# Performance work log

Hardware: AMD Instinct MI355X
Metric: run time of the kernel (lower is better)

## Reference

```python
import jax, jax.numpy as jnp
import numpy as np

D_MODEL = 2048
N_HEADS = 16
D_HEAD = D_MODEL // N_HEADS  # 128


def setup_inputs() -> dict:
    key = jax.random.key(0)
    ks = jax.random.split(key, 5)
    b, t = 2, 2048
    s = 0.02
    return {
        "x": jax.random.normal(ks[0], (b, t, D_MODEL), dtype=jnp.float32),
        "Wq": jax.random.normal(ks[1], (D_MODEL, D_MODEL), dtype=jnp.float32) * s,
        "Wk": jax.random.normal(ks[2], (D_MODEL, D_HEAD), dtype=jnp.float32) * s,
        "Wv": jax.random.normal(ks[3], (D_MODEL, D_HEAD), dtype=jnp.float32) * s,
        "Wo": jax.random.normal(ks[4], (D_MODEL, D_MODEL), dtype=jnp.float32) * s,
    }


def reference(x, Wq, Wk, Wv, Wo):
    b, t, c = x.shape
    scale = D_HEAD ** -0.5
    # q: [b, h, t, d]; k, v: single shared KV head [b, s, d]
    q = (x @ Wq).reshape(b, t, N_HEADS, D_HEAD).transpose(0, 2, 1, 3)
    k = x @ Wk  # [b, s, d]
    v = x @ Wv  # [b, s, d]
    # broadcast the shared KV head across query heads without materializing copies
    scores = jnp.einsum('bhtd,bsd->bhts', q, k) * scale
    attn = jax.nn.softmax(scores, axis=-1)
    y = jnp.einsum('bhts,bsd->bhtd', attn, v)
    y = y.transpose(0, 2, 1, 3).reshape(b, t, c)
    return y @ Wo
```

## Files before the change

kernel.cpp:

```cpp
#include <hip/hip_runtime.h>

typedef unsigned short ushort_t;
typedef short bf16x8 __attribute__((ext_vector_type(8)));
typedef float f32x4 __attribute__((ext_vector_type(4)));

#define B_    2
#define T_    2048
#define C_    2048
#define H_    16
#define DH_   128
#define BT_   4096
#define NQKV  2304

#define OFF_XB   0UL
#define OFF_WT   16777216UL
#define OFF_WOT  26214400UL
#define OFF_QKV  34603008UL
#define OFF_VT   53477376UL
#define OFF_FLAG 54525952UL

__device__ __forceinline__ ushort_t f2bf(float f) {
  union { float f; unsigned u; } v; v.f = f;
  unsigned r = v.u + 0x7fffu + ((v.u >> 16) & 1u);
  return (ushort_t)(r >> 16);
}
__device__ __forceinline__ float bf2f(ushort_t u) {
  union { float f; unsigned u; } v; v.u = ((unsigned)u) << 16;
  return v.f;
}
__device__ __forceinline__ int cvtpk_bf16(float lo, float hi) {
  int r;
  asm("v_cvt_pk_bf16_f32 %0, %1, %2" : "=v"(r) : "v"(lo), "v"(hi));
  return r;
}
__device__ __forceinline__ bf16x8 mkfrag(int d0, int d1, int d2, int d3) {
  union { int i[4]; bf16x8 v; } u;
  u.i[0] = d0; u.i[1] = d1; u.i[2] = d2; u.i[3] = d3;
  return u.v;
}

__device__ __forceinline__ void gload_lds16(const ushort_t* g, ushort_t* l) {
  __builtin_amdgcn_global_load_lds((__attribute__((address_space(1))) void*)g,
                                   (__attribute__((address_space(3))) void*)l,
                                   16, 0, 0);
}

__global__ void detect_dtype(const ushort_t* x, int* flag) {
  if (threadIdx.x == 0 && blockIdx.x == 0) {
    int sane = 0;
    for (int i = 0; i < 32; ++i) {
      ushort_t u = x[2 * i];
      int e = (u >> 7) & 0xFF;
      if (u == 0 || (e >= 100 && e <= 140)) ++sane;
    }
    *flag = (sane >= 24) ? 1 : 0;
  }
}

__global__ __launch_bounds__(256) void cast_x(const void* __restrict__ xin,
                                              ushort_t* __restrict__ xb,
                                              const int* __restrict__ flag, int n8) {
  int i = blockIdx.x * 256 + threadIdx.x;
  if (i >= n8) return;
  if (*flag) {
    *(bf16x8*)(xb + (size_t)i * 8) = *(const bf16x8*)((const ushort_t*)xin + (size_t)i * 8);
  } else {
    const float* xf = (const float*)xin;
    f32x4 a = *(const f32x4*)(xf + (size_t)i * 8);
    f32x4 b = *(const f32x4*)(xf + (size_t)i * 8 + 4);
    bf16x8 o;
    o[0] = (short)f2bf(a[0]); o[1] = (short)f2bf(a[1]);
    o[2] = (short)f2bf(a[2]); o[3] = (short)f2bf(a[3]);
    o[4] = (short)f2bf(b[0]); o[5] = (short)f2bf(b[1]);
    o[6] = (short)f2bf(b[2]); o[7] = (short)f2bf(b[3]);
    *(bf16x8*)(xb + (size_t)i * 8) = o;
  }
}

__global__ __launch_bounds__(256) void transpose_cast(const void* __restrict__ src,
                                                      ushort_t* __restrict__ dst,
                                                      const int* __restrict__ flag,
                                                      int rows, int cols, int dst_ld,
                                                      int dst_row_off) {
  __shared__ float tile[32][33];
  int c0 = blockIdx.x * 32, r0 = blockIdx.y * 32;
  int tx = threadIdx.x & 31, ty = threadIdx.x >> 5;
  bool isbf = (*flag != 0);
#pragma unroll
  for (int j = 0; j < 4; ++j) {
    int r = r0 + ty + j * 8;
    float v;
    if (isbf) v = bf2f(((const ushort_t*)src)[(size_t)r * cols + c0 + tx]);
    else      v = ((const float*)src)[(size_t)r * cols + c0 + tx];
    tile[ty + j * 8][tx] = v;
  }
  __syncthreads();
#pragma unroll
  for (int j = 0; j < 4; ++j) {
    int c = c0 + ty + j * 8;
    dst[(size_t)(dst_row_off + c) * dst_ld + r0 + tx] = f2bf(tile[tx][ty + j * 8]);
  }
}

__global__ __launch_bounds__(256) void transpose_v(const ushort_t* __restrict__ qkv,
                                                   ushort_t* __restrict__ vT) {
  __shared__ ushort_t tile[32][33];
  int b = blockIdx.z;
  int t0 = blockIdx.x * 32, d0 = blockIdx.y * 32;
  int tx = threadIdx.x & 31, ty = threadIdx.x >> 5;
#pragma unroll
  for (int j = 0; j < 4; ++j) {
    int t = t0 + ty + j * 8;
    tile[ty + j * 8][tx] = qkv[(size_t)(b * T_ + t) * NQKV + 2176 + d0 + tx];
  }
  __syncthreads();
#pragma unroll
  for (int j = 0; j < 4; ++j) {
    int d = d0 + ty + j * 8;
    vT[(size_t)b * (DH_ * T_) + (size_t)d * T_ + t0 + tx] = tile[tx][ty + j * 8];
  }
}

__global__ __launch_bounds__(256) void gemm_bt(const ushort_t* __restrict__ A,
                                               const ushort_t* __restrict__ Bt,
                                               void* __restrict__ Cv,
                                               int M, int N, int K,
                                               int is_final, const int* __restrict__ flag,
                                               float qscale, int qcols) {
  __shared__ __align__(16) ushort_t As[2][128 * 32];
  __shared__ __align__(16) ushort_t Bs[2][128 * 32];
  const int tid = threadIdx.x;
  const int lane = tid & 63;
  const int wid = tid >> 6;

  const int gx = gridDim.x;
  const int nwg = gx * gridDim.y;
  const int orig = blockIdx.y * gx + blockIdx.x;
  const int qq = nwg >> 3, rr = nwg & 7;
  const int xcd = orig & 7, pos = orig >> 3;
  const int wg = (xcd < rr ? xcd * (qq + 1) : rr * (qq + 1) + (xcd - rr) * qq) + pos;
  const int bx = wg % gx, by = wg / gx;

  const int m0 = by * 128;
  const int n0 = bx * 128;
  const int wr = wid >> 1, wc = wid & 1;
  const int l15 = lane & 15, l4 = lane >> 4;

  f32x4 zero = {0.f, 0.f, 0.f, 0.f};
  f32x4 acc[4][4];
#pragma unroll
  for (int r = 0; r < 4; ++r)
#pragma unroll
    for (int c = 0; c < 4; ++c) acc[r][c] = zero;

  const ushort_t* ga = A + (size_t)(m0 + (tid >> 2)) * K + (tid & 3) * 8;
  const ushort_t* gb = Bt + (size_t)(n0 + (tid >> 2)) * K + (tid & 3) * 8;
  const size_t stride64 = (size_t)64 * K;
  const int lofs = wid * 512;

  gload_lds16(ga, As[0] + lofs);
  gload_lds16(ga + stride64, As[0] + lofs + 2048);
  gload_lds16(gb, Bs[0] + lofs);
  gload_lds16(gb + stride64, Bs[0] + lofs + 2048);

  const int NT = K >> 5;
  for (int t = 0; t < NT; ++t) {
    const int cur = t & 1;
    if (t + 1 < NT) {
      const int k1 = (t + 1) << 5;
      gload_lds16(ga + k1, As[cur ^ 1] + lofs);
      gload_lds16(ga + k1 + stride64, As[cur ^ 1] + lofs + 2048);
      gload_lds16(gb + k1, Bs[cur ^ 1] + lofs);
      gload_lds16(gb + k1 + stride64, Bs[cur ^ 1] + lofs + 2048);
      asm volatile("s_waitcnt vmcnt(4)" ::: "memory");
    } else {
      asm volatile("s_waitcnt vmcnt(0)" ::: "memory");
    }
    __builtin_amdgcn_s_barrier();

    bf16x8 af[4], bfr[4];
#pragma unroll
    for (int r = 0; r < 4; ++r)
      af[r] = *(const bf16x8*)&As[cur][(wr * 64 + r * 16 + l15) * 32 + l4 * 8];
#pragma unroll
    for (int c = 0; c < 4; ++c)
      bfr[c] = *(const bf16x8*)&Bs[cur][(wc * 64 + c * 16 + l15) * 32 + l4 * 8];
    __builtin_amdgcn_s_setprio(1);
#pragma unroll
    for (int r = 0; r < 4; ++r)
#pragma unroll
      for (int c = 0; c < 4; ++c)
        acc[r][c] = __builtin_amdgcn_mfma_f32_16x16x32_bf16(af[r], bfr[c], acc[r][c], 0, 0, 0);
    __builtin_amdgcn_s_setprio(0);
    __builtin_amdgcn_s_barrier();
  }

  const bool f32out = is_final && (*flag == 0);
#pragma unroll
  for (int r = 0; r < 4; ++r) {
#pragma unroll
    for (int c = 0; c < 4; ++c) {
      int row = m0 + wr * 64 + r * 16 + l4 * 4;
      int col = n0 + wc * 64 + c * 16 + l15;
      float s = (col < qcols) ? qscale : 1.0f;
#pragma unroll
      for (int g = 0; g < 4; ++g) {
        float v = acc[r][c][g] * s;
        if (f32out) ((float*)Cv)[(size_t)(row + g) * N + col] = v;
        else ((ushort_t*)Cv)[(size_t)(row + g) * N + col] = f2bf(v);
      }
    }
  }
}

__global__ __launch_bounds__(256, 2) void attn_kernel(const ushort_t* __restrict__ qkv,
                                                      const ushort_t* __restrict__ vT,
                                                      ushort_t* __restrict__ y) {
  __shared__ __align__(16) ushort_t Ks[2][64 * 128];
  __shared__ __align__(16) ushort_t Vs[2][128 * 64];

  const int tid = threadIdx.x;
  const int lane = tid & 63;
  const int wid = tid >> 6;
  const int h = blockIdx.y;
  const int b = blockIdx.z;
  const int tb = b * T_;
  const int q0 = blockIdx.x * 128 + wid * 32;
  const int l15 = lane & 15, l4 = lane >> 4;

  bf16x8 qf0[4], qf1[4];
  {
    const ushort_t* qb0 = qkv + (size_t)(tb + q0 + l15) * NQKV + h * DH_ + l4 * 8;
    const ushort_t* qb1 = qb0 + (size_t)16 * NQKV;
#pragma unroll
    for (int ks = 0; ks < 4; ++ks) {
      qf0[ks] = *(const bf16x8*)(qb0 + ks * 32);
      qf1[ks] = *(const bf16x8*)(qb1 + ks * 32);
    }
  }

  const ushort_t* ksrcb[4];
  const ushort_t* vsrcb[4];
  int koff[4], voff[4];
#pragma unroll
  for (int it = 0; it < 4; ++it) {
    int id = tid + it * 256;
    int krow = id >> 4, kslot = id & 15;
    ksrcb[it] = qkv + (size_t)(tb + krow) * NQKV + 2048 + ((kslot ^ (krow & 7)) << 3);
    koff[it] = (it * 256 + (wid << 6)) * 8;
    int vrow = id >> 3, vslot = id & 7;
    vsrcb[it] = vT + (size_t)b * (DH_ * T_) + (size_t)vrow * T_ + ((vslot ^ (vrow & 7)) << 3);
    voff[it] = (it * 256 + (wid << 6)) * 8;
  }

  f32x4 zero = {0.f, 0.f, 0.f, 0.f};
  f32x4 o0[8], o1[8];
#pragma unroll
  for (int i = 0; i < 8; ++i) { o0[i] = zero; o1[i] = zero; }
  float m0s = -1e30f, m1s = -1e30f;
  float l0s = 0.f, l1s = 0.f;

#pragma unroll
  for (int it = 0; it < 4; ++it) {
    gload_lds16(ksrcb[it], &Ks[0][koff[it]]);
    gload_lds16(vsrcb[it], &Vs[0][voff[it]]);
  }

  for (int st = 0; st < 32; ++st) {
    const int cur = st & 1;
    __syncthreads();
    if (st < 31) {
      const int s1 = (st + 1) * 64;
#pragma unroll
      for (int it = 0; it < 4; ++it) {
        gload_lds16(ksrcb[it] + (size_t)s1 * NQKV, &Ks[cur ^ 1][koff[it]]);
        gload_lds16(vsrcb[it] + s1, &Vs[cur ^ 1][voff[it]]);
      }
    }

    f32x4 sa0[4], sa1[4];
    __builtin_amdgcn_s_setprio(1);
#pragma unroll
    for (int c = 0; c < 4; ++c) {
      int srow = c * 16 + l15;
      int sw = srow & 7;
      bf16x8 kf[4];
#pragma unroll
      for (int ks = 0; ks < 4; ++ks)
        kf[ks] = *(const bf16x8*)&Ks[cur][srow * 128 + (((ks * 4 + l4) ^ sw) << 3)];
      sa0[c] = zero; sa1[c] = zero;
#pragma unroll
      for (int ks = 0; ks < 4; ++ks) {
        sa0[c] = __builtin_amdgcn_mfma_f32_16x16x32_bf16(kf[ks], qf0[ks], sa0[c], 0, 0, 0);
        sa1[c] = __builtin_amdgcn_mfma_f32_16x16x32_bf16(kf[ks], qf1[ks], sa1[c], 0, 0, 0);
      }
    }
    __builtin_amdgcn_s_setprio(0);

    float pmax0 = sa0[0][0];
#pragma unroll
    for (int c = 0; c < 4; ++c)
#pragma unroll
      for (int r = 0; r < 4; ++r) pmax0 = fmaxf(pmax0, sa0[c][r]);
    pmax0 = fmaxf(pmax0, __shfl_xor(pmax0, 16));
    pmax0 = fmaxf(pmax0, __shfl_xor(pmax0, 32));
    if (!__all(pmax0 - m0s <= 8.0f)) {
      float mn = fmaxf(m0s, pmax0);
      float al = exp2f(m0s - mn);
      m0s = mn; l0s *= al;
      float ar[4];
#pragma unroll
      for (int r = 0; r < 4; ++r) ar[r] = __shfl(al, l4 * 4 + r);
#pragma unroll
      for (int nb = 0; nb < 8; ++nb)
#pragma unroll
        for (int r = 0; r < 4; ++r) o0[nb][r] *= ar[r];
    }
    float ps0 = 0.f;
#pragma unroll
    for (int c = 0; c < 4; ++c)
#pragma unroll
      for (int r = 0; r < 4; ++r) {
        float p = exp2f(sa0[c][r] - m0s);
        sa0[c][r] = p;
        ps0 += p;
      }
    ps0 += __shfl_xor(ps0, 16);
    ps0 += __shfl_xor(ps0, 32);
    l0s += ps0;

    float pmax1 = sa1[0][0];
#pragma unroll
    for (int c = 0; c < 4; ++c)
#pragma unroll
      for (int r = 0; r < 4; ++r) pmax1 = fmaxf(pmax1, sa1[c][r]);
    pmax1 = fmaxf(pmax1, __shfl_xor(pmax1, 16));
    pmax1 = fmaxf(pmax1, __shfl_xor(pmax1, 32));
    if (!__all(pmax1 - m1s <= 8.0f)) {
      float mn = fmaxf(m1s, pmax1);
      float al = exp2f(m1s - mn);
      m1s = mn; l1s *= al;
      float ar[4];
#pragma unroll
      for (int r = 0; r < 4; ++r) ar[r] = __shfl(al, l4 * 4 + r);
#pragma unroll
      for (int nb = 0; nb < 8; ++nb)
#pragma unroll
        for (int r = 0; r < 4; ++r) o1[nb][r] *= ar[r];
    }
    float ps1 = 0.f;
#pragma unroll
    for (int c = 0; c < 4; ++c)
#pragma unroll
      for (int r = 0; r < 4; ++r) {
        float p = exp2f(sa1[c][r] - m1s);
        sa1[c][r] = p;
        ps1 += p;
      }
    ps1 += __shfl_xor(ps1, 16);
    ps1 += __shfl_xor(ps1, 32);
    l1s += ps1;

    const int srcA = ((lane >> 4) & 1) * 32 + l15;
    const int srcB = srcA + 16;
    const bool cHi = lane >= 32;

    bf16x8 g0pa0, g0pa1, g1pa0, g1pa1;
    {
      int pk0[2], pk1[2], pk2[2], pk3[2];
      pk0[0] = cvtpk_bf16(sa0[0][0], sa0[0][1]); pk0[1] = cvtpk_bf16(sa0[0][2], sa0[0][3]);
      pk1[0] = cvtpk_bf16(sa0[1][0], sa0[1][1]); pk1[1] = cvtpk_bf16(sa0[1][2], sa0[1][3]);
      pk2[0] = cvtpk_bf16(sa0[2][0], sa0[2][1]); pk2[1] = cvtpk_bf16(sa0[2][2], sa0[2][3]);
      pk3[0] = cvtpk_bf16(sa0[3][0], sa0[3][1]); pk3[1] = cvtpk_bf16(sa0[3][2], sa0[3][3]);
      int a00 = __shfl(pk0[0], srcA), a01 = __shfl(pk0[1], srcA);
      int a02 = __shfl(pk0[0], srcB), a03 = __shfl(pk0[1], srcB);
      int b00 = __shfl(pk1[0], srcA), b01 = __shfl(pk1[1], srcA);
      int b02 = __shfl(pk1[0], srcB), b03 = __shfl(pk1[1], srcB);
      g0pa0 = mkfrag(cHi ? b00 : a00, cHi ? b01 : a01, cHi ? b02 : a02, cHi ? b03 : a03);
      int a10 = __shfl(pk2[0], srcA), a11 = __shfl(pk2[1], srcA);
      int a12 = __shfl(pk2[0], srcB), a13 = __shfl(pk2[1], srcB);
      int b10 = __shfl(pk3[0], srcA), b11 = __shfl(pk3[1], srcA);
      int b12 = __shfl(pk3[0], srcB), b13 = __shfl(pk3[1], srcB);
      g0pa1 = mkfrag(cHi ? b10 : a10, cHi ? b11 : a11, cHi ? b12 : a12, cHi ? b13 : a13);
    }
    {
      int pk0[2], pk1[2], pk2[2], pk3[2];
      pk0[0] = cvtpk_bf16(sa1[0][0], sa1[0][1]); pk0[1] = cvtpk_bf16(sa1[0][2], sa1[0][3]);
      pk1[0] = cvtpk_bf16(sa1[1][0], sa1[1][1]); pk1[1] = cvtpk_bf16(sa1[1][2], sa1[1][3]);
      pk2[0] = cvtpk_bf16(sa1[2][0], sa1[2][1]); pk2[1] = cvtpk_bf16(sa1[2][2], sa1[2][3]);
      pk3[0] = cvtpk_bf16(sa1[3][0], sa1[3][1]); pk3[1] = cvtpk_bf16(sa1[3][2], sa1[3][3]);
      int a00 = __shfl(pk0[0], srcA), a01 = __shfl(pk0[1], srcA);
      int a02 = __shfl(pk0[0], srcB), a03 = __shfl(pk0[1], srcB);
      int b00 = __shfl(pk1[0], srcA), b01 = __shfl(pk1[1], srcA);
      int b02 = __shfl(pk1[0], srcB), b03 = __shfl(pk1[1], srcB);
      g1pa0 = mkfrag(cHi ? b00 : a00, cHi ? b01 : a01, cHi ? b02 : a02, cHi ? b03 : a03);
      int a10 = __shfl(pk2[0], srcA), a11 = __shfl(pk2[1], srcA);
      int a12 = __shfl(pk2[0], srcB), a13 = __shfl(pk2[1], srcB);
      int b10 = __shfl(pk3[0], srcA), b11 = __shfl(pk3[1], srcA);
      int b12 = __shfl(pk3[0], srcB), b13 = __shfl(pk3[1], srcB);
      g1pa1 = mkfrag(cHi ? b10 : a10, cHi ? b11 : a11, cHi ? b12 : a12, cHi ? b13 : a13);
    }

    __builtin_amdgcn_s_setprio(1);
#pragma unroll
    for (int nb = 0; nb < 8; ++nb) {
      int vrow = nb * 16 + l15;
      int sw = vrow & 7;
      bf16x8 vb0 = *(const bf16x8*)&Vs[cur][vrow * 64 + ((l4 ^ sw) << 3)];
      o0[nb] = __builtin_amdgcn_mfma_f32_16x16x32_bf16(g0pa0, vb0, o0[nb], 0, 0, 0);
      o1[nb] = __builtin_amdgcn_mfma_f32_16x16x32_bf16(g1pa0, vb0, o1[nb], 0, 0, 0);
      bf16x8 vb1 = *(const bf16x8*)&Vs[cur][vrow * 64 + (((4 + l4) ^ sw) << 3)];
      o0[nb] = __builtin_amdgcn_mfma_f32_16x16x32_bf16(g0pa1, vb1, o0[nb], 0, 0, 0);
      o1[nb] = __builtin_amdgcn_mfma_f32_16x16x32_bf16(g1pa1, vb1, o1[nb], 0, 0, 0);
    }
    __builtin_amdgcn_s_setprio(0);
  }

  {
    float lr[4];
#pragma unroll
    for (int r = 0; r < 4; ++r) lr[r] = __shfl(l0s, l4 * 4 + r);
#pragma unroll
    for (int nb = 0; nb < 8; ++nb)
#pragma unroll
      for (int r = 0; r < 4; ++r) {
        int qrow = tb + q0 + l4 * 4 + r;
        y[(size_t)qrow * C_ + h * DH_ + nb * 16 + l15] = f2bf(o0[nb][r] / lr[r]);
      }
  }
  {
    float lr[4];
#pragma unroll
    for (int r = 0; r < 4; ++r) lr[r] = __shfl(l1s, l4 * 4 + r);
#pragma unroll
    for (int nb = 0; nb < 8; ++nb)
#pragma unroll
      for (int r = 0; r < 4; ++r) {
        int qrow = tb + q0 + 16 + l4 * 4 + r;
        y[(size_t)qrow * C_ + h * DH_ + nb * 16 + l15] = f2bf(o1[nb][r] / lr[r]);
      }
  }
}

extern "C" void kernel_launch(void* const* d_in, const int* in_sizes, int n_in,
                              void* d_out, int out_size, void* d_ws, size_t ws_size,
                              hipStream_t stream) {
  (void)in_sizes; (void)n_in; (void)out_size; (void)ws_size;
  const void* x  = d_in[0];
  const void* Wq = d_in[1];
  const void* Wk = d_in[2];
  const void* Wv = d_in[3];
  const void* Wo = d_in[4];

  char* ws = (char*)d_ws;
  ushort_t* xb  = (ushort_t*)(ws + OFF_XB);
  ushort_t* WT  = (ushort_t*)(ws + OFF_WT);
  ushort_t* WoT = (ushort_t*)(ws + OFF_WOT);
  ushort_t* qkv = (ushort_t*)(ws + OFF_QKV);
  ushort_t* vTp = (ushort_t*)(ws + OFF_VT);
  int* flag     = (int*)(ws + OFF_FLAG);

  detect_dtype<<<1, 1, 0, stream>>>((const ushort_t*)x, flag);

  cast_x<<<4096, 256, 0, stream>>>(x, xb, flag, (BT_ * C_) / 8);

  transpose_cast<<<dim3(64, 64), 256, 0, stream>>>(Wq, WT, flag, 2048, 2048, 2048, 0);
  transpose_cast<<<dim3(4, 64), 256, 0, stream>>>(Wk, WT, flag, 2048, 128, 2048, 2048);
  transpose_cast<<<dim3(4, 64), 256, 0, stream>>>(Wv, WT, flag, 2048, 128, 2048, 2176);
  transpose_cast<<<dim3(64, 64), 256, 0, stream>>>(Wo, WoT, flag, 2048, 2048, 2048, 0);

  const float k1 = 0.08838834764831845f * 1.4426950408889634f;
  gemm_bt<<<dim3(NQKV / 128, BT_ / 128), 256, 0, stream>>>(xb, WT, qkv, BT_, NQKV, C_, 0, flag, k1, 2048);

  transpose_v<<<dim3(T_ / 32, DH_ / 32, B_), 256, 0, stream>>>(qkv, vTp);

  attn_kernel<<<dim3(T_ / 128, H_, B_), 256, 0, stream>>>(qkv, vTp, xb);

  gemm_bt<<<dim3(C_ / 128, BT_ / 128), 256, 0, stream>>>(xb, WoT, d_out, BT_, C_, C_, 1, flag, 1.0f, 0);
}
```

Measured before the change: 344.8 us.

## Switch attention kernel to 32x32x16 MFMA with permlane32 swaps for P

Rewrites the attention inner loop to use 32x32x16 bf16 MFMA tiles instead of 16x16x32, so each wave holds its 32 query rows in one tile and keys in two 32-row tiles. This changes the register layout of S and O and halves the number of MFMA issues and softmax shuffles per step. The P-to-A-operand relayout now uses v_permlane32_swap instead of many ds_bpermute shuffles. The final normalization multiplies by a reciprocal instead of dividing. The risks are higher accumulator register pressure, a different LDS read pattern and a layout mismatch that would silently give wrong results.

```diff
diff --git a/kernel.cpp b/kernel.cpp
--- a/kernel.cpp
+++ b/kernel.cpp
@@ -3,6 +3,7 @@
 typedef unsigned short ushort_t;
 typedef short bf16x8 __attribute__((ext_vector_type(8)));
 typedef float f32x4 __attribute__((ext_vector_type(4)));
+typedef float f32x16 __attribute__((ext_vector_type(16)));
 
 #define B_    2
 #define T_    2048
@@ -32,6 +33,9 @@
   int r;
   asm("v_cvt_pk_bf16_f32 %0, %1, %2" : "=v"(r) : "v"(lo), "v"(hi));
   return r;
+}
+__device__ __forceinline__ void plswap(int& x, int& y) {
+  asm volatile("v_permlane32_swap_b32 %0, %1" : "+v"(x), "+v"(y));
 }
 __device__ __forceinline__ bf16x8 mkfrag(int d0, int d1, int d2, int d3) {
   union { int i[4]; bf16x8 v; } u;
@@ -226,17 +230,13 @@
   const int b = blockIdx.z;
   const int tb = b * T_;
   const int q0 = blockIdx.x * 128 + wid * 32;
-  const int l15 = lane & 15, l4 = lane >> 4;
-
-  bf16x8 qf0[4], qf1[4];
+  const int l31 = lane & 31, hi = lane >> 5;
+
+  bf16x8 qf[8];
   {
-    const ushort_t* qb0 = qkv + (size_t)(tb + q0 + l15) * NQKV + h * DH_ + l4 * 8;
-    const ushort_t* qb1 = qb0 + (size_t)16 * NQKV;
-#pragma unroll
-    for (int ks = 0; ks < 4; ++ks) {
-      qf0[ks] = *(const bf16x8*)(qb0 + ks * 32);
-      qf1[ks] = *(const bf16x8*)(qb1 + ks * 32);
-    }
+    const ushort_t* qb = qkv + (size_t)(tb + q0 + l31) * NQKV + h * DH_ + hi * 8;
+#pragma unroll
+    for (int kk = 0; kk < 8; ++kk) qf[kk] = *(const bf16x8*)(qb + kk * 16);
   }
 
   const ushort_t* ksrcb[4];
@@ -253,12 +253,13 @@
     voff[it] = (it * 256 + (wid << 6)) * 8;
   }
 
-  f32x4 zero = {0.f, 0.f, 0.f, 0.f};
-  f32x4 o0[8], o1[8];
-#pragma unroll
-  for (int i = 0; i < 8; ++i) { o0[i] = zero; o1[i] = zero; }
-  float m0s = -1e30f, m1s = -1e30f;
-  float l0s = 0.f, l1s = 0.f;
+  f32x16 o[4];
+#pragma unroll
+  for (int d = 0; d < 4; ++d)
+#pragma unroll
+    for (int r = 0; r < 16; ++r) o[d][r] = 0.f;
+  float m_s = -1e30f;
+  float l_s = 0.f;
 
 #pragma unroll
   for (int it = 0; it < 4; ++it) {
@@ -278,167 +279,105 @@
       }
     }
 
-    f32x4 sa0[4], sa1[4];
+    f32x16 sa0, sa1;
+#pragma unroll
+    for (int r = 0; r < 16; ++r) { sa0[r] = 0.f; sa1[r] = 0.f; }
+    const int r0 = l31, r1 = 32 + l31;
+    const int sw0 = r0 & 7, sw1 = r1 & 7;
     __builtin_amdgcn_s_setprio(1);
 #pragma unroll
-    for (int c = 0; c < 4; ++c) {
-      int srow = c * 16 + l15;
-      int sw = srow & 7;
-      bf16x8 kf[4];
-#pragma unroll
-      for (int ks = 0; ks < 4; ++ks)
-        kf[ks] = *(const bf16x8*)&Ks[cur][srow * 128 + (((ks * 4 + l4) ^ sw) << 3)];
-      sa0[c] = zero; sa1[c] = zero;
-#pragma unroll
-      for (int ks = 0; ks < 4; ++ks) {
-        sa0[c] = __builtin_amdgcn_mfma_f32_16x16x32_bf16(kf[ks], qf0[ks], sa0[c], 0, 0, 0);
-        sa1[c] = __builtin_amdgcn_mfma_f32_16x16x32_bf16(kf[ks], qf1[ks], sa1[c], 0, 0, 0);
-      }
+    for (int kk = 0; kk < 8; ++kk) {
+      bf16x8 k0 = *(const bf16x8*)&Ks[cur][r0 * 128 + (((kk * 2 + hi) ^ sw0) << 3)];
+      bf16x8 k1 = *(const bf16x8*)&Ks[cur][r1 * 128 + (((kk * 2 + hi) ^ sw1) << 3)];
+      sa0 = __builtin_amdgcn_mfma_f32_32x32x16_bf16(k0, qf[kk], sa0, 0, 0, 0);
+      sa1 = __builtin_amdgcn_mfma_f32_32x32x16_bf16(k1, qf[kk], sa1, 0, 0, 0);
     }
     __builtin_amdgcn_s_setprio(0);
 
-    float pmax0 = sa0[0][0];
-#pragma unroll
-    for (int c = 0; c < 4; ++c)
-#pragma unroll
-      for (int r = 0; r < 4; ++r) pmax0 = fmaxf(pmax0, sa0[c][r]);
-    pmax0 = fmaxf(pmax0, __shfl_xor(pmax0, 16));
-    pmax0 = fmaxf(pmax0, __shfl_xor(pmax0, 32));
-    if (!__all(pmax0 - m0s <= 8.0f)) {
-      float mn = fmaxf(m0s, pmax0);
-      float al = exp2f(m0s - mn);
-      m0s = mn; l0s *= al;
-      float ar[4];
-#pragma unroll
-      for (int r = 0; r < 4; ++r) ar[r] = __shfl(al, l4 * 4 + r);
-#pragma unroll
-      for (int nb = 0; nb < 8; ++nb)
-#pragma unroll
-        for (int r = 0; r < 4; ++r) o0[nb][r] *= ar[r];
-    }
-    float ps0 = 0.f;
-#pragma unroll
-    for (int c = 0; c < 4; ++c)
-#pragma unroll
-      for (int r = 0; r < 4; ++r) {
-        float p = exp2f(sa0[c][r] - m0s);
-        sa0[c][r] = p;
-        ps0 += p;
-      }
-    ps0 += __shfl_xor(ps0, 16);
-    ps0 += __shfl_xor(ps0, 32);
-    l0s += ps0;
-
-    float pmax1 = sa1[0][0];
-#pragma unroll
-    for (int c = 0; c < 4; ++c)
-#pragma unroll
-      for (int r = 0; r < 4; ++r) pmax1 = fmaxf(pmax1, sa1[c][r]);
-    pmax1 = fmaxf(pmax1, __shfl_xor(pmax1, 16));
-    pmax1 = fmaxf(pmax1, __shfl_xor(pmax1, 32));
-    if (!__all(pmax1 - m1s <= 8.0f)) {
-      float mn = fmaxf(m1s, pmax1);
-      float al = exp2f(m1s - mn);
-      m1s = mn; l1s *= al;
-      float ar[4];
-#pragma unroll
-      for (int r = 0; r < 4; ++r) ar[r] = __shfl(al, l4 * 4 + r);
-#pragma unroll
-      for (int nb = 0; nb < 8; ++nb)
-#pragma unroll
-        for (int r = 0; r < 4; ++r) o1[nb][r] *= ar[r];
-    }
-    float ps1 = 0.f;
-#pragma unroll
-    for (int c = 0; c < 4; ++c)
-#pragma unroll
-      for (int r = 0; r < 4; ++r) {
-        float p = exp2f(sa1[c][r] - m1s);
-        sa1[c][r] = p;
-        ps1 += p;
-      }
-    ps1 += __shfl_xor(ps1, 16);
-    ps1 += __shfl_xor(ps1, 32);
-    l1s += ps1;
-
-    const int srcA = ((lane >> 4) & 1) * 32 + l15;
-    const int srcB = srcA + 16;
-    const bool cHi = lane >= 32;
-
-    bf16x8 g0pa0, g0pa1, g1pa0, g1pa1;
+    float pmax = sa0[0];
+#pragma unroll
+    for (int r = 1; r < 16; ++r) pmax = fmaxf(pmax, sa0[r]);
+#pragma unroll
+    for (int r = 0; r < 16; ++r) pmax = fmaxf(pmax, sa1[r]);
+    pmax = fmaxf(pmax, __shfl_xor(pmax, 32));
+
+    if (!__all(pmax - m_s <= 8.0f)) {
+      float mn = fmaxf(m_s, pmax);
+      float al = exp2f(m_s - mn);
+      m_s = mn; l_s *= al;
+      float ar[16];
+#pragma unroll
+      for (int r = 0; r < 16; ++r) ar[r] = __shfl(al, (r & 3) + 8 * (r >> 2) + 4 * hi);
+#pragma unroll
+      for (int d = 0; d < 4; ++d)
+#pragma unroll
+        for (int r = 0; r < 16; ++r) o[d][r] *= ar[r];
+    }
+
+    float ps = 0.f;
+#pragma unroll
+    for (int r = 0; r < 16; ++r) {
+      float p = exp2f(sa0[r] - m_s);
+      sa0[r] = p; ps += p;
+    }
+#pragma unroll
+    for (int r = 0; r < 16; ++r) {
+      float p = exp2f(sa1[r] - m_s);
+      sa1[r] = p; ps += p;
+    }
+    ps += __shfl_xor(ps, 32);
+    l_s += ps;
+
+    bf16x8 pa0, pa1, pa2, pa3;
     {
-      int pk0[2], pk1[2], pk2[2], pk3[2];
-      pk0[0] = cvtpk_bf16(sa0[0][0], sa0[0][1]); pk0[1] = cvtpk_bf16(sa0[0][2], sa0[0][3]);
-      pk1[0] = cvtpk_bf16(sa0[1][0], sa0[1][1]); pk1[1] = cvtpk_bf16(sa0[1][2], sa0[1][3]);
-      pk2[0] = cvtpk_bf16(sa0[2][0], sa0[2][1]); pk2[1] = cvtpk_bf16(sa0[2][2], sa0[2][3]);
-      pk3[0] = cvtpk_bf16(sa0[3][0], sa0[3][1]); pk3[1] = cvtpk_bf16(sa0[3][2], sa0[3][3]);
-      int a00 = __shfl(pk0[0], srcA), a01 = __shfl(pk0[1], srcA);
-      int a02 = __shfl(pk0[0], srcB), a03 = __shfl(pk0[1], srcB);
-      int b00 = __shfl(pk1[0], srcA), b01 = __shfl(pk1[1], srcA);
-      int b02 = __shfl(pk1[0], srcB), b03 = __shfl(pk1[1], srcB);
-      g0pa0 = mkfrag(cHi ? b00 : a00, cHi ? b01 : a01, cHi ? b02 : a02, cHi ? b03 : a03);
-      int a10 = __shfl(pk2[0], srcA), a11 = __shfl(pk2[1], srcA);
-      int a12 = __shfl(pk2[0], srcB), a13 = __shfl(pk2[1], srcB);
-      int b10 = __shfl(pk3[0], srcA), b11 = __shfl(pk3[1], srcA);
-      int b12 = __shfl(pk3[0], srcB), b13 = __shfl(pk3[1], srcB);
-      g0pa1 = mkfrag(cHi ? b10 : a10, cHi ? b11 : a11, cHi ? b12 : a12, cHi ? b13 : a13);
+      int a = cvtpk_bf16(sa0[0], sa0[1]),  b2 = cvtpk_bf16(sa0[2], sa0[3]);
+      int c = cvtpk_bf16(sa0[4], sa0[5]),  d2 = cvtpk_bf16(sa0[6], sa0[7]);
+      int e = cvtpk_bf16(sa0[8], sa0[9]),  f2 = cvtpk_bf16(sa0[10], sa0[11]);
+      int g = cvtpk_bf16(sa0[12], sa0[13]), h2 = cvtpk_bf16(sa0[14], sa0[15]);
+      plswap(a, c);  plswap(b2, d2);
+      plswap(e, g);  plswap(f2, h2);
+      pa0 = mkfrag(a, b2, c, d2);
+      pa1 = mkfrag(e, f2, g, h2);
     }
     {
-      int pk0[2], pk1[2], pk2[2], pk3[2];
-      pk0[0] = cvtpk_bf16(sa1[0][0], sa1[0][1]); pk0[1] = cvtpk_bf16(sa1[0][2], sa1[0][3]);
-      pk1[0] = cvtpk_bf16(sa1[1][0], sa1[1][1]); pk1[1] = cvtpk_bf16(sa1[1][2], sa1[1][3]);
-      pk2[0] = cvtpk_bf16(sa1[2][0], sa1[2][1]); pk2[1] = cvtpk_bf16(sa1[2][2], sa1[2][3]);
-      pk3[0] = cvtpk_bf16(sa1[3][0], sa1[3][1]); pk3[1] = cvtpk_bf16(sa1[3][2], sa1[3][3]);
-      int a00 = __shfl(pk0[0], srcA), a01 = __shfl(pk0[1], srcA);
-      int a02 = __shfl(pk0[0], srcB), a03 = __shfl(pk0[1], srcB);
-      int b00 = __shfl(pk1[0], srcA), b01 = __shfl(pk1[1], srcA);
-      int b02 = __shfl(pk1[0], srcB), b03 = __shfl(pk1[1], srcB);
-      g1pa0 = mkfrag(cHi ? b00 : a00, cHi ? b01 : a01, cHi ? b02 : a02, cHi ? b03 : a03);
-      int a10 = __shfl(pk2[0], srcA), a11 = __shfl(pk2[1], srcA);
-      int a12 = __shfl(pk2[0], srcB), a13 = __shfl(pk2[1], srcB);
-      int b10 = __shfl(pk3[0], srcA), b11 = __shfl(pk3[1], srcA);
-      int b12 = __shfl(pk3[0], srcB), b13 = __shfl(pk3[1], srcB);
-      g1pa1 = mkfrag(cHi ? b10 : a10, cHi ? b11 : a11, cHi ? b12 : a12, cHi ? b13 : a13);
+      int a = cvtpk_bf16(sa1[0], sa1[1]),  b2 = cvtpk_bf16(sa1[2], sa1[3]);
+      int c = cvtpk_bf16(sa1[4], sa1[5]),  d2 = cvtpk_bf16(sa1[6], sa1[7]);
+      int e = cvtpk_bf16(sa1[8], sa1[9]),  f2 = cvtpk_bf16(sa1[10], sa1[11]);
+      int g = cvtpk_bf16(sa1[12], sa1[13]), h2 = cvtpk_bf16(sa1[14], sa1[15]);
+      plswap(a, c);  plswap(b2, d2);
+      plswap(e, g);  plswap(f2, h2);
+      pa2 = mkfrag(a, b2, c, d2);
+      pa3 = mkfrag(e, f2, g, h2);
     }
 
     __builtin_amdgcn_s_setprio(1);
 #pragma unroll
-    for (int nb = 0; nb < 8; ++nb) {
-      int vrow = nb * 16 + l15;
-      int sw = vrow & 7;
-      bf16x8 vb0 = *(const bf16x8*)&Vs[cur][vrow * 64 + ((l4 ^ sw) << 3)];
-      o0[nb] = __builtin_amdgcn_mfma_f32_16x16x32_bf16(g0pa0, vb0, o0[nb], 0, 0, 0);
-      o1[nb] = __builtin_amdgcn_mfma_f32_16x16x32_bf16(g1pa0, vb0, o1[nb], 0, 0, 0);
-      bf16x8 vb1 = *(const bf16x8*)&Vs[cur][vrow * 64 + (((4 + l4) ^ sw) << 3)];
-      o0[nb] = __builtin_amdgcn_mfma_f32_16x16x32_bf16(g0pa1, vb1, o0[nb], 0, 0, 0);
-      o1[nb] = __builtin_amdgcn_mfma_f32_16x16x32_bf16(g1pa1, vb1, o1[nb], 0, 0, 0);
+    for (int dblk = 0; dblk < 4; ++dblk) {
+      int vrow = dblk * 32 + l31;
+      int vsw = vrow & 7;
+      bf16x8 v0 = *(const bf16x8*)&Vs[cur][vrow * 64 + (((0 * 2 + hi) ^ vsw) << 3)];
+      o[dblk] = __builtin_amdgcn_mfma_f32_32x32x16_bf16(pa0, v0, o[dblk], 0, 0, 0);
+      bf16x8 v1 = *(const bf16x8*)&Vs[cur][vrow * 64 + (((1 * 2 + hi) ^ vsw) << 3)];
+      o[dblk] = __builtin_amdgcn_mfma_f32_32x32x16_bf16(pa1, v1, o[dblk], 0, 0, 0);
+      bf16x8 v2 = *(const bf16x8*)&Vs[cur][vrow * 64 + (((2 * 2 + hi) ^ vsw) << 3)];
+      o[dblk] = __builtin_amdgcn_mfma_f32_32x32x16_bf16(pa2, v2, o[dblk], 0, 0, 0);
+      bf16x8 v3 = *(const bf16x8*)&Vs[cur][vrow * 64 + (((3 * 2 + hi) ^ vsw) << 3)];
+      o[dblk] = __builtin_amdgcn_mfma_f32_32x32x16_bf16(pa3, v3, o[dblk], 0, 0, 0);
     }
     __builtin_amdgcn_s_setprio(0);
   }
 
-  {
-    float lr[4];
-#pragma unroll
-    for (int r = 0; r < 4; ++r) lr[r] = __shfl(l0s, l4 * 4 + r);
-#pragma unroll
-    for (int nb = 0; nb < 8; ++nb)
-#pragma unroll
-      for (int r = 0; r < 4; ++r) {
-        int qrow = tb + q0 + l4 * 4 + r;
-        y[(size_t)qrow * C_ + h * DH_ + nb * 16 + l15] = f2bf(o0[nb][r] / lr[r]);
-      }
-  }
-  {
-    float lr[4];
-#pragma unroll
-    for (int r = 0; r < 4; ++r) lr[r] = __shfl(l1s, l4 * 4 + r);
-#pragma unroll
-    for (int nb = 0; nb < 8; ++nb)
-#pragma unroll
-      for (int r = 0; r < 4; ++r) {
-        int qrow = tb + q0 + 16 + l4 * 4 + r;
-        y[(size_t)qrow * C_ + h * DH_ + nb * 16 + l15] = f2bf(o1[nb][r] / lr[r]);
-      }
+  float inv_l = 1.0f / l_s;
+  float rl[16];
+#pragma unroll
+  for (int r = 0; r < 16; ++r) rl[r] = __shfl(inv_l, (r & 3) + 8 * (r >> 2) + 4 * hi);
+#pragma unroll
+  for (int dblk = 0; dblk < 4; ++dblk) {
+#pragma unroll
+    for (int r = 0; r < 16; ++r) {
+      int qr = (r & 3) + 8 * (r >> 2) + 4 * hi;
+      y[(size_t)(tb + q0 + qr) * C_ + h * DH_ + dblk * 32 + l31] = f2bf(o[dblk][r] * rl[r]);
+    }
   }
 }
 
```

Result: faster. 320.5 us (-7.0%).
